# Optimization experiments

Hardware: AMD Instinct MI355X
Metric: run time of the kernel (lower is better)

The kernel has to match this reference:

```python
import jax, jax.numpy as jnp
import numpy as np

N_NODES = 50000
N_EDGES = 800000
D = 128           # 2 * hidden_channels
N_LAYERS = 9
N_GRAPHS = 256
EPS = 1e-05


def setup_inputs() -> dict:
    key = jax.random.key(0)
    ks = jax.random.split(key, 12)
    x = jax.random.normal(ks[0], (N_NODES, 13), dtype=jnp.float32)
    edge_index = jax.random.randint(ks[1], (2, N_EDGES), 0, N_NODES, dtype=jnp.int64)
    edge_attr = jax.random.normal(ks[2], (N_EDGES, 4), dtype=jnp.float32)
    batch = jnp.sort(jax.random.randint(ks[3], (N_NODES,), 0, N_GRAPHS, dtype=jnp.int64))
    s13 = 1.0 / np.sqrt(13)
    s4 = 1.0 / np.sqrt(4)
    sD = 1.0 / np.sqrt(D)
    s512 = 1.0 / np.sqrt(512)
    Wv = jax.random.uniform(ks[4], (13, D), jnp.float32, -s13, s13)
    We = jax.random.uniform(ks[5], (4, D), jnp.float32, -s4, s4)
    conv_w = jax.random.uniform(ks[6], (N_LAYERS, D, D), jnp.float32, -sD, sD)
    conv_b = jax.random.uniform(ks[7], (N_LAYERS, D), jnp.float32, -sD, sD)
    Wh1 = jax.random.uniform(ks[8], (D, 512), jnp.float32, -sD, sD)
    bh1 = jax.random.uniform(ks[9], (512,), jnp.float32, -sD, sD)
    Wh2 = jax.random.uniform(ks[10], (512, 1), jnp.float32, -s512, s512)
    bh2 = jax.random.uniform(ks[11], (1,), jnp.float32, -s512, s512)
    return {"x": x, "edge_index": edge_index, "edge_attr": edge_attr, "batch": batch,
            "Wv": Wv, "We": We, "conv_w": conv_w, "conv_b": conv_b,
            "Wh1": Wh1, "bh1": bh1, "Wh2": Wh2, "bh2": bh2}


def reference(x, edge_index, edge_attr, batch, Wv, We, conv_w, conv_b, Wh1, bh1, Wh2, bh2):
    src, dst = edge_index[0], edge_index[1]
    h = x @ Wv                      # [N, D]
    ea = edge_attr @ We             # [E, D]

    def layer(h, wb):
        W, b = wb
        msg = jax.nn.relu(h[src] + ea)                     # [E, D] gather + elementwise
        aggr = jax.ops.segment_sum(msg, dst, num_segments=N_NODES)  # scatter-add
        out = ((1.0 + EPS) * h + aggr) @ W + b             # GINEConv nn (Linear)
        return jax.nn.relu(out) + h, None                  # residual

    h, _ = jax.lax.scan(layer, h, (conv_w, conv_b))

    # global mean pool over graphs
    sums = jax.ops.segment_sum(h, batch, num_segments=N_GRAPHS)    # [G, D]
    cnt = jax.ops.segment_sum(jnp.ones((h.shape[0],), h.dtype), batch, num_segments=N_GRAPHS)
    pooled = sums / jnp.maximum(cnt, 1.0)[:, None]

    out = jax.nn.gelu(pooled @ Wh1 + bh1, approximate=False) @ Wh2 + bh2  # [G, 1]
    return out
```

## Files before the change

kernel.cpp:

```cpp
#include <hip/hip_runtime.h>
#include <math.h>

#define N_NODES 50000
#define N_EDGES 800000
#define DCH 128
#define N_LAYERS 9
#define N_GRAPHS 256
#define EPSF 1e-5f
#define NCHUNK 196
#define NSLICE 4
#define SL_SZ 12500

typedef __attribute__((ext_vector_type(8))) short short8;
typedef __attribute__((ext_vector_type(4))) float floatx4;

static __device__ __forceinline__ unsigned short f2bf(float f) {
    unsigned int u = __float_as_uint(f);
    unsigned int r = (u + 0x7fffu + ((u >> 16) & 1u)) >> 16;
    return (unsigned short)r;
}
static __device__ __forceinline__ unsigned int pack_bf2(float a, float b) {
    return (unsigned int)f2bf(a) | ((unsigned int)f2bf(b) << 16);
}
static __device__ __forceinline__ float bflo(unsigned int u) { return __uint_as_float(u << 16); }
static __device__ __forceinline__ float bfhi(unsigned int u) { return __uint_as_float(u & 0xffff0000u); }

static __device__ __forceinline__ float dot2bf(unsigned int a, unsigned int b, float c) {
    float d;
    asm("v_dot2_f32_bf16 %0, %1, %2, %3" : "=v"(d) : "v"(a), "v"(b), "v"(c));
    return d;
}

static __device__ __forceinline__ int dbucket(int d) { return 63 - min(d, 63); }

__global__ void hist_kernel(const int* __restrict__ dst, int* __restrict__ deg) {
    int t = blockIdx.x * 256 + threadIdx.x;
    atomicAdd(&deg[dst[t]], 1);
}

__global__ __launch_bounds__(256) void dsort_hist_kernel(const int* __restrict__ deg,
                                                         int* __restrict__ bhist) {
    __shared__ int lh[64];
    int t = threadIdx.x;
    if (t < 64) lh[t] = 0;
    __syncthreads();
    int n = blockIdx.x * 256 + t;
    if (n < N_NODES) atomicAdd(&lh[dbucket(deg[n])], 1);
    __syncthreads();
    if (t < 64) bhist[blockIdx.x * 64 + t] = lh[t];
}

__global__ __launch_bounds__(64) void dsort_scan_kernel(const int* __restrict__ bhist,
                                                        int* __restrict__ boff) {
    __shared__ int tot[64];
    __shared__ int base[64];
    int b = threadIdx.x;
    int s = 0;
    for (int blk = 0; blk < NCHUNK; blk++) s += bhist[blk * 64 + b];
    tot[b] = s;
    __syncthreads();
    if (b == 0) {
        int run = 0;
        for (int i = 0; i < 64; i++) { base[i] = run; run += tot[i]; }
    }
    __syncthreads();
    int run = base[b];
    for (int blk = 0; blk < NCHUNK; blk++) {
        boff[blk * 64 + b] = run;
        run += bhist[blk * 64 + b];
    }
}

__global__ __launch_bounds__(256) void dsort_scatter_kernel(const int* __restrict__ deg,
                                                            const int* __restrict__ boff,
                                                            int* __restrict__ nperm,
                                                            int* __restrict__ inv) {
    __shared__ int cur[64];
    int t = threadIdx.x;
    if (t < 64) cur[t] = boff[blockIdx.x * 64 + t];
    __syncthreads();
    int n = blockIdx.x * 256 + t;
    if (n < N_NODES) {
        int p = atomicAdd(&cur[dbucket(deg[n])], 1);
        nperm[p] = n;
        inv[n] = p;
    }
}

__global__ void dstinv_kernel(const int* __restrict__ dst, const int* __restrict__ inv,
                              int* __restrict__ dstinv) {
    int t = blockIdx.x * 256 + threadIdx.x;
    dstinv[t] = inv[dst[t]];
}

__global__ __launch_bounds__(256) void chunksum_kernel(const int* __restrict__ deg,
                                                       const int* __restrict__ nperm,
                                                       int* __restrict__ csum) {
    int t = threadIdx.x;
    int i = blockIdx.x * 256 + t;
    int v = (i < N_NODES) ? deg[nperm[i]] : 0;
    __shared__ int sh[4];
    for (int off = 32; off >= 1; off >>= 1) v += __shfl_down(v, off);
    if ((t & 63) == 0) sh[t >> 6] = v;
    __syncthreads();
    if (t == 0) csum[blockIdx.x] = sh[0] + sh[1] + sh[2] + sh[3];
}

__global__ __launch_bounds__(256) void chunkscan_kernel(const int* __restrict__ csum,
                                                        int* __restrict__ coff) {
    __shared__ int sh[256];
    int t = threadIdx.x;
    sh[t] = (t < NCHUNK) ? csum[t] : 0;
    __syncthreads();
    for (int off = 1; off < 256; off <<= 1) {
        int v = (t >= off) ? sh[t - off] : 0;
        __syncthreads();
        sh[t] += v;
        __syncthreads();
    }
    if (t < NCHUNK) coff[t] = t ? sh[t - 1] : 0;
}

__global__ __launch_bounds__(256) void applyscan_kernel(const int* __restrict__ deg,
                                                        const int* __restrict__ nperm,
                                                        const int* __restrict__ coff,
                                                        int* __restrict__ rowp,
                                                        int* __restrict__ cursor) {
    __shared__ int sh[256];
    int t = threadIdx.x;
    int i = blockIdx.x * 256 + t;
    int d = (i < N_NODES) ? deg[nperm[i]] : 0;
    sh[t] = d;
    __syncthreads();
    for (int off = 1; off < 256; off <<= 1) {
        int v = (t >= off) ? sh[t - off] : 0;
        __syncthreads();
        sh[t] += v;
        __syncthreads();
    }
    int excl = coff[blockIdx.x] + (t ? sh[t - 1] : 0);
    if (i < N_NODES) {
        rowp[i] = excl;
        cursor[i] = excl;
    }
    if (i == N_NODES - 1) rowp[N_NODES] = N_EDGES;
}

__global__ __launch_bounds__(256) void scatter_kernel(const int* __restrict__ src,
                                                      const int* __restrict__ dstinv,
                                                      const int* __restrict__ inv,
                                                      const float* __restrict__ eattr,
                                                      int* __restrict__ cursor,
                                                      uint4* __restrict__ erec) {
    int s = blockIdx.x & (NSLICE - 1);
    int chunk = blockIdx.x / NSLICE;
    int e0 = chunk * 1024 + threadIdx.x * 4;
    if (e0 >= N_EDGES) return;
    int4 d4 = *(const int4*)(dstinv + e0);
#pragma unroll
    for (int k = 0; k < 4; k++) {
        int e = e0 + k;
        int d = (k == 0) ? d4.x : (k == 1) ? d4.y : (k == 2) ? d4.z : d4.w;
        if (d / SL_SZ == s) {
            int p = atomicAdd(&cursor[d], 1);
            float4 a = ((const float4*)eattr)[e];
            erec[p] = make_uint4((unsigned int)inv[src[e]],
                                 pack_bf2(a.x, a.y), pack_bf2(a.z, a.w), 0u);
        }
    }
}

__global__ __launch_bounds__(256) void wconv_kernel(const float* __restrict__ convW,
                                                    uint4* __restrict__ wb) {
    int tid = blockIdx.x * 256 + threadIdx.x;
    int lane = tid & 63;
    int t = (tid >> 6) & 31;
    int layer = tid >> 11;
    int jt = t >> 2, kt = t & 3;
    int quad = lane >> 4, col = lane & 15;
    const float* Wl = convW + (size_t)layer * DCH * DCH;
    int kbase = kt * 32 + quad * 8;
    int ch = jt * 16 + col;
    unsigned int d0 = pack_bf2(Wl[(kbase + 0) * DCH + ch], Wl[(kbase + 1) * DCH + ch]);
    unsigned int d1 = pack_bf2(Wl[(kbase + 2) * DCH + ch], Wl[(kbase + 3) * DCH + ch]);
    unsigned int d2 = pack_bf2(Wl[(kbase + 4) * DCH + ch], Wl[(kbase + 5) * DCH + ch]);
    unsigned int d3 = pack_bf2(Wl[(kbase + 6) * DCH + ch], Wl[(kbase + 7) * DCH + ch]);
    wb[tid] = make_uint4(d0, d1, d2, d3);
}

__global__ void h0_kernel(const float* __restrict__ x, const float* __restrict__ Wv,
                          const int* __restrict__ inv,
                          float* __restrict__ h, unsigned int* __restrict__ hbf) {
    int t = blockIdx.x * 256 + threadIdx.x;
    int n = t >> 6, l = t & 63;
    const float* xr = x + n * 13;
    float s0 = 0.f, s1 = 0.f;
#pragma unroll
    for (int j = 0; j < 13; j++) {
        float xv = xr[j];
        s0 = fmaf(xv, Wv[j * 128 + 2 * l], s0);
        s1 = fmaf(xv, Wv[j * 128 + 2 * l + 1], s1);
    }
    int p = inv[n];
    ((float2*)h)[(size_t)p * 64 + l] = make_float2(s0, s1);
    hbf[(size_t)p * 64 + l] = pack_bf2(s0, s1);
}

#define VSTRIDE 68
#define OLP 132
__global__ __launch_bounds__(256) void layer_kernel(const float* __restrict__ hin,
                                                    const unsigned int* __restrict__ hbfA,
                                                    const uint4* __restrict__ erec,
                                                    const int* __restrict__ rowp,
                                                    const float* __restrict__ We,
                                                    const short8* __restrict__ wbL,
                                                    const float* __restrict__ b,
                                                    float* __restrict__ hout,
                                                    unsigned int* __restrict__ hbfB,
                                                    int write_hbf) {
    __shared__ unsigned int vsh[16 * VSTRIDE];
    __shared__ float ol[16 * OLP];
    __shared__ float2 hsh[16 * 64];
    int tid = threadIdx.x;
    int lane = tid & 63;
    int wave = tid >> 6;
    int nb = blockIdx.x * 16;
    unsigned int wy0 = pack_bf2(We[0 * 128 + 2 * lane], We[1 * 128 + 2 * lane]);
    unsigned int wz0 = pack_bf2(We[2 * 128 + 2 * lane], We[3 * 128 + 2 * lane]);
    unsigned int wy1 = pack_bf2(We[0 * 128 + 2 * lane + 1], We[1 * 128 + 2 * lane + 1]);
    unsigned int wz1 = pack_bf2(We[2 * 128 + 2 * lane + 1], We[3 * 128 + 2 * lane + 1]);
    const float2* h2 = (const float2*)hin;
    for (int j = 0; j < 4; j++) {
        int nl = wave * 4 + j;
        int n = nb + nl;
        int start = rowp[n], end = rowp[n + 1];
        float a0 = 0.f, a1 = 0.f;
        int e = start;
        for (; e + 4 <= end; e += 4) {
            uint4 r0 = erec[e], r1 = erec[e + 1], r2 = erec[e + 2], r3 = erec[e + 3];
            unsigned int u0 = hbfA[r0.x * 64u + (unsigned)lane];
            unsigned int u1 = hbfA[r1.x * 64u + (unsigned)lane];
            unsigned int u2 = hbfA[r2.x * 64u + (unsigned)lane];
            unsigned int u3 = hbfA[r3.x * 64u + (unsigned)lane];
            float p0 = dot2bf(r0.y, wy0, dot2bf(r0.z, wz0, 0.f));
            float p1 = dot2bf(r0.y, wy1, dot2bf(r0.z, wz1, 0.f));
            float q0 = dot2bf(r1.y, wy0, dot2bf(r1.z, wz0, 0.f));
            float q1 = dot2bf(r1.y, wy1, dot2bf(r1.z, wz1, 0.f));
            float s0 = dot2bf(r2.y, wy0, dot2bf(r2.z, wz0, 0.f));
            float s1 = dot2bf(r2.y, wy1, dot2bf(r2.z, wz1, 0.f));
            float t0 = dot2bf(r3.y, wy0, dot2bf(r3.z, wz0, 0.f));
            float t1 = dot2bf(r3.y, wy1, dot2bf(r3.z, wz1, 0.f));
            a0 += fmaxf(bflo(u0) + p0, 0.f);
            a1 += fmaxf(bfhi(u0) + p1, 0.f);
            a0 += fmaxf(bflo(u1) + q0, 0.f);
            a1 += fmaxf(bfhi(u1) + q1, 0.f);
            a0 += fmaxf(bflo(u2) + s0, 0.f);
            a1 += fmaxf(bfhi(u2) + s1, 0.f);
            a0 += fmaxf(bflo(u3) + t0, 0.f);
            a1 += fmaxf(bfhi(u3) + t1, 0.f);
        }
        for (; e < end; e++) {
            uint4 r0 = erec[e];
            unsigned int u0 = hbfA[r0.x * 64u + (unsigned)lane];
            float p0 = dot2bf(r0.y, wy0, dot2bf(r0.z, wz0, 0.f));
            float p1 = dot2bf(r0.y, wy1, dot2bf(r0.z, wz1, 0.f));
            a0 += fmaxf(bflo(u0) + p0, 0.f);
            a1 += fmaxf(bfhi(u0) + p1, 0.f);
        }
        float2 hn = h2[(size_t)n * 64 + lane];
        hsh[nl * 64 + lane] = hn;
        float vx = fmaf(hn.x, 1.f + EPSF, a0);
        float vy = fmaf(hn.y, 1.f + EPSF, a1);
        vsh[nl * VSTRIDE + lane] = pack_bf2(vx, vy);
    }
    __syncthreads();
    int col = lane & 15, quad = lane >> 4;
    short8 a[4];
#pragma unroll
    for (int kt = 0; kt < 4; kt++) {
        a[kt] = *(const short8*)(vsh + col * VSTRIDE + kt * 16 + quad * 4);
    }
#pragma unroll
    for (int jj = 0; jj < 2; jj++) {
        int jt = wave * 2 + jj;
        floatx4 acc = {0.f, 0.f, 0.f, 0.f};
#pragma unroll
        for (int kt = 0; kt < 4; kt++) {
            short8 bf = wbL[(jt * 4 + kt) * 64 + lane];
            acc = __builtin_amdgcn_mfma_f32_16x16x32_bf16(a[kt], bf, acc, 0, 0, 0);
        }
        float bv = b[jt * 16 + col];
#pragma unroll
        for (int r = 0; r < 4; r++) {
            ol[(quad * 4 + r) * OLP + jt * 16 + col] = fmaxf(acc[r] + bv, 0.f);
        }
    }
    __syncthreads();
    float4* o4 = (float4*)hout;
    uint2* b2 = (uint2*)hbfB;
#pragma unroll
    for (int i = 0; i < 2; i++) {
        int idx = i * 256 + tid;
        int nl = idx >> 5, c4 = idx & 31;
        int node = nb + nl;
        const float* row = ol + nl * OLP + c4 * 4;
        float2 h01 = hsh[nl * 64 + 2 * c4];
        float2 h23 = hsh[nl * 64 + 2 * c4 + 1];
        float4 r;
        r.x = row[0] + h01.x;
        r.y = row[1] + h01.y;
        r.z = row[2] + h23.x;
        r.w = row[3] + h23.y;
        o4[(size_t)node * 32 + c4] = r;
        if (write_hbf)
            b2[(size_t)node * 32 + c4] = make_uint2(pack_bf2(r.x, r.y), pack_bf2(r.z, r.w));
    }
}

__global__ void bounds_kernel(const int* __restrict__ batch, int* __restrict__ gs) {
    int n = blockIdx.x * 256 + threadIdx.x;
    if (n >= N_NODES) return;
    int bcur = batch[n];
    int prev = (n == 0) ? -1 : batch[n - 1];
    for (int g = prev + 1; g <= bcur; g++) gs[g] = n;
    if (n == N_NODES - 1) {
        for (int g = bcur + 1; g <= N_GRAPHS; g++) gs[g] = N_NODES;
    }
}

__global__ __launch_bounds__(256) void pool_kernel(const float* __restrict__ h,
                                                   const int* __restrict__ inv,
                                                   const int* __restrict__ batch,
                                                   float* __restrict__ sums) {
    int wave = threadIdx.x >> 6, l = threadIdx.x & 63;
    int nbase = (blockIdx.x * 4 + wave) * 8;
    const float2* h2 = (const float2*)h;
    float a0 = 0.f, a1 = 0.f;
    int g = -1;
#pragma unroll
    for (int i = 0; i < 8; i++) {
        int n = nbase + i;
        if (n >= N_NODES) break;
        int bg = batch[n];
        if (bg != g) {
            if (g >= 0) {
                atomicAdd(&sums[g * 128 + 2 * l], a0);
                atomicAdd(&sums[g * 128 + 2 * l + 1], a1);
            }
            g = bg; a0 = 0.f; a1 = 0.f;
        }
        int p = inv[n];
        float2 hv = h2[(size_t)p * 64 + l];
        a0 += hv.x; a1 += hv.y;
    }
    if (g >= 0) {
        atomicAdd(&sums[g * 128 + 2 * l], a0);
        atomicAdd(&sums[g * 128 + 2 * l + 1], a1);
    }
}

__global__ __launch_bounds__(512) void mlp_kernel(const float* __restrict__ sums,
                                                  const int* __restrict__ gs,
                                                  const float* __restrict__ Wh1,
                                                  const float* __restrict__ bh1,
                                                  const float* __restrict__ Wh2,
                                                  const float* __restrict__ bh2,
                                                  float* __restrict__ out) {
    int g = blockIdx.x;
    __shared__ float pl[128];
    __shared__ float red[8];
    int tid = threadIdx.x;
    if (tid < 128) {
        float cnt = fmaxf((float)(gs[g + 1] - gs[g]), 1.0f);
        pl[tid] = sums[g * 128 + tid] / cnt;
    }
    __syncthreads();
    float s = bh1[tid];
#pragma unroll 16
    for (int k = 0; k < 128; k++) s = fmaf(pl[k], Wh1[k * 512 + tid], s);
    float gl = 0.5f * s * (1.0f + erff(s * 0.70710678118654752f));
    float p = gl * Wh2[tid];
    for (int off = 32; off >= 1; off >>= 1) p += __shfl_down(p, off);
    if ((tid & 63) == 0) red[tid >> 6] = p;
    __syncthreads();
    if (tid == 0) {
        float tot = 0.f;
        for (int i = 0; i < 8; i++) tot += red[i];
        out[g] = tot + bh2[0];
    }
}

extern "C" void kernel_launch(void* const* d_in, const int* in_sizes, int n_in,
                              void* d_out, int out_size, void* d_ws, size_t ws_size,
                              hipStream_t stream) {
    const float* x = (const float*)d_in[0];
    const int* ei = (const int*)d_in[1];
    const float* eattr = (const float*)d_in[2];
    const int* batch = (const int*)d_in[3];
    const float* Wv = (const float*)d_in[4];
    const float* We = (const float*)d_in[5];
    const float* convW = (const float*)d_in[6];
    const float* convB = (const float*)d_in[7];
    const float* Wh1 = (const float*)d_in[8];
    const float* bh1 = (const float*)d_in[9];
    const float* Wh2 = (const float*)d_in[10];
    const float* bh2 = (const float*)d_in[11];
    float* out = (float*)d_out;

    const int* src = ei;
    const int* dst = ei + N_EDGES;

    char* w = (char*)d_ws;
    size_t off = 0;
    auto alloc = [&](size_t bytes) -> char* {
        char* p = w + off;
        off += (bytes + 255) & ~(size_t)255;
        return p;
    };
    float* bufA = (float*)alloc((size_t)N_NODES * DCH * 4);
    float* bufB = (float*)alloc((size_t)N_NODES * DCH * 4);
    unsigned int* hbfA = (unsigned int*)alloc((size_t)N_NODES * 64 * 4);
    unsigned int* hbfB = (unsigned int*)alloc((size_t)N_NODES * 64 * 4);
    uint4* wb = (uint4*)alloc((size_t)N_LAYERS * 32 * 64 * 16);
    int* deg = (int*)alloc((size_t)(N_NODES + 1) * 4);
    int* rowp = (int*)alloc((size_t)(N_NODES + 1) * 4);
    int* cursor = (int*)alloc((size_t)(N_NODES + 1) * 4);
    int* csum = (int*)alloc((size_t)NCHUNK * 4);
    int* coff = (int*)alloc((size_t)NCHUNK * 4);
    int* bhist = (int*)alloc((size_t)NCHUNK * 64 * 4);
    int* boff = (int*)alloc((size_t)NCHUNK * 64 * 4);
    int* nperm = (int*)alloc((size_t)N_NODES * 4);
    int* inv = (int*)alloc((size_t)N_NODES * 4);
    int* dstinv = (int*)alloc((size_t)N_EDGES * 4);
    uint4* erec = (uint4*)alloc((size_t)N_EDGES * 16);
    int* gs = (int*)alloc((size_t)(N_GRAPHS + 1) * 4);
    float* sums = (float*)alloc((size_t)N_GRAPHS * DCH * 4);
    (void)ws_size; (void)n_in; (void)in_sizes; (void)out_size;

    hipMemsetAsync(deg, 0, (size_t)(N_NODES + 1) * 4, stream);
    hipMemsetAsync(sums, 0, (size_t)N_GRAPHS * DCH * 4, stream);

    hist_kernel<<<N_EDGES / 256, 256, 0, stream>>>(dst, deg);
    dsort_hist_kernel<<<NCHUNK, 256, 0, stream>>>(deg, bhist);
    dsort_scan_kernel<<<1, 64, 0, stream>>>(bhist, boff);
    dsort_scatter_kernel<<<NCHUNK, 256, 0, stream>>>(deg, boff, nperm, inv);
    dstinv_kernel<<<N_EDGES / 256, 256, 0, stream>>>(dst, inv, dstinv);
    chunksum_kernel<<<NCHUNK, 256, 0, stream>>>(deg, nperm, csum);
    chunkscan_kernel<<<1, 256, 0, stream>>>(csum, coff);
    applyscan_kernel<<<NCHUNK, 256, 0, stream>>>(deg, nperm, coff, rowp, cursor);
    scatter_kernel<<<782 * NSLICE, 256, 0, stream>>>(src, dstinv, inv, eattr, cursor, erec);
    wconv_kernel<<<72, 256, 0, stream>>>(convW, wb);
    h0_kernel<<<N_NODES * 64 / 256, 256, 0, stream>>>(x, Wv, inv, bufA, hbfA);
    bounds_kernel<<<(N_NODES + 255) / 256, 256, 0, stream>>>(batch, gs);

    float* hcur = bufA;
    float* hnext = bufB;
    unsigned int* bfcur = hbfA;
    unsigned int* bfnext = hbfB;
    for (int layer = 0; layer < N_LAYERS; layer++) {
        layer_kernel<<<N_NODES / 16, 256, 0, stream>>>(
            hcur, bfcur, erec, rowp, We,
            (const short8*)(wb + (size_t)layer * 2048), convB + (size_t)layer * DCH,
            hnext, bfnext, (layer < N_LAYERS - 1) ? 1 : 0);
        float* t = hcur; hcur = hnext; hnext = t;
        unsigned int* tb = bfcur; bfcur = bfnext; bfnext = tb;
    }

    pool_kernel<<<(N_NODES + 31) / 32, 256, 0, stream>>>(hcur, inv, batch, sums);
    mlp_kernel<<<N_GRAPHS, 512, 0, stream>>>(sums, gs, Wh1, bh1, Wh2, bh2, out);
}
```

Baseline: 696.1 us.

## Flatten per-wave edge loop across four nodes with 8-wide prefetched gathers

Each wave now walks the concatenated edge range of its four destination nodes as one stream, processing 8 edges per iteration and prefetching the next 8 edge records while the current gathers are in flight. Accumulators are flushed into shared memory whenever a node boundary is crossed. Row pointers go through readfirstlane and the four h rows are loaded up front. Launch bounds now request 5 blocks per CU. The goal is more memory-level parallelism and less tail-loop overhead for low-degree nodes, at the cost of higher register pressure and per-edge boundary checks.

```diff
diff --git a/kernel.cpp b/kernel.cpp
--- a/kernel.cpp
+++ b/kernel.cpp
@@ -208,16 +208,16 @@
 
 #define VSTRIDE 68
 #define OLP 132
-__global__ __launch_bounds__(256) void layer_kernel(const float* __restrict__ hin,
-                                                    const unsigned int* __restrict__ hbfA,
-                                                    const uint4* __restrict__ erec,
-                                                    const int* __restrict__ rowp,
-                                                    const float* __restrict__ We,
-                                                    const short8* __restrict__ wbL,
-                                                    const float* __restrict__ b,
-                                                    float* __restrict__ hout,
-                                                    unsigned int* __restrict__ hbfB,
-                                                    int write_hbf) {
+__global__ __launch_bounds__(256, 5) void layer_kernel(const float* __restrict__ hin,
+                                                       const unsigned int* __restrict__ hbfA,
+                                                       const uint4* __restrict__ erec,
+                                                       const int* __restrict__ rowp,
+                                                       const float* __restrict__ We,
+                                                       const short8* __restrict__ wbL,
+                                                       const float* __restrict__ b,
+                                                       float* __restrict__ hout,
+                                                       unsigned int* __restrict__ hbfB,
+                                                       int write_hbf) {
     __shared__ unsigned int vsh[16 * VSTRIDE];
     __shared__ float ol[16 * OLP];
     __shared__ float2 hsh[16 * 64];
@@ -230,49 +230,95 @@
     unsigned int wy1 = pack_bf2(We[0 * 128 + 2 * lane + 1], We[1 * 128 + 2 * lane + 1]);
     unsigned int wz1 = pack_bf2(We[2 * 128 + 2 * lane + 1], We[3 * 128 + 2 * lane + 1]);
     const float2* h2 = (const float2*)hin;
-    for (int j = 0; j < 4; j++) {
-        int nl = wave * 4 + j;
-        int n = nb + nl;
-        int start = rowp[n], end = rowp[n + 1];
-        float a0 = 0.f, a1 = 0.f;
-        int e = start;
-        for (; e + 4 <= end; e += 4) {
-            uint4 r0 = erec[e], r1 = erec[e + 1], r2 = erec[e + 2], r3 = erec[e + 3];
-            unsigned int u0 = hbfA[r0.x * 64u + (unsigned)lane];
-            unsigned int u1 = hbfA[r1.x * 64u + (unsigned)lane];
-            unsigned int u2 = hbfA[r2.x * 64u + (unsigned)lane];
-            unsigned int u3 = hbfA[r3.x * 64u + (unsigned)lane];
-            float p0 = dot2bf(r0.y, wy0, dot2bf(r0.z, wz0, 0.f));
-            float p1 = dot2bf(r0.y, wy1, dot2bf(r0.z, wz1, 0.f));
-            float q0 = dot2bf(r1.y, wy0, dot2bf(r1.z, wz0, 0.f));
-            float q1 = dot2bf(r1.y, wy1, dot2bf(r1.z, wz1, 0.f));
-            float s0 = dot2bf(r2.y, wy0, dot2bf(r2.z, wz0, 0.f));
-            float s1 = dot2bf(r2.y, wy1, dot2bf(r2.z, wz1, 0.f));
-            float t0 = dot2bf(r3.y, wy0, dot2bf(r3.z, wz0, 0.f));
-            float t1 = dot2bf(r3.y, wy1, dot2bf(r3.z, wz1, 0.f));
-            a0 += fmaxf(bflo(u0) + p0, 0.f);
-            a1 += fmaxf(bfhi(u0) + p1, 0.f);
-            a0 += fmaxf(bflo(u1) + q0, 0.f);
-            a1 += fmaxf(bfhi(u1) + q1, 0.f);
-            a0 += fmaxf(bflo(u2) + s0, 0.f);
-            a1 += fmaxf(bfhi(u2) + s1, 0.f);
-            a0 += fmaxf(bflo(u3) + t0, 0.f);
-            a1 += fmaxf(bfhi(u3) + t1, 0.f);
+
+    int n0 = nb + wave * 4;
+    int b0 = __builtin_amdgcn_readfirstlane(rowp[n0]);
+    int b1 = __builtin_amdgcn_readfirstlane(rowp[n0 + 1]);
+    int b2 = __builtin_amdgcn_readfirstlane(rowp[n0 + 2]);
+    int b3 = __builtin_amdgcn_readfirstlane(rowp[n0 + 3]);
+    int b4 = __builtin_amdgcn_readfirstlane(rowp[n0 + 4]);
+
+    float2 hn0 = h2[(size_t)(n0 + 0) * 64 + lane];
+    float2 hn1 = h2[(size_t)(n0 + 1) * 64 + lane];
+    float2 hn2 = h2[(size_t)(n0 + 2) * 64 + lane];
+    float2 hn3 = h2[(size_t)(n0 + 3) * 64 + lane];
+    hsh[(wave * 4 + 0) * 64 + lane] = hn0;
+    hsh[(wave * 4 + 1) * 64 + lane] = hn1;
+    hsh[(wave * 4 + 2) * 64 + lane] = hn2;
+    hsh[(wave * 4 + 3) * 64 + lane] = hn3;
+
+    float c0 = 0.f, c1 = 0.f;
+    int nl = 0;
+    int bq = b1;
+
+    auto FLUSH = [&]() {
+        float hx = (nl == 0) ? hn0.x : (nl == 1) ? hn1.x : (nl == 2) ? hn2.x : hn3.x;
+        float hy = (nl == 0) ? hn0.y : (nl == 1) ? hn1.y : (nl == 2) ? hn2.y : hn3.y;
+        float vx = fmaf(hx, 1.f + EPSF, c0);
+        float vy = fmaf(hy, 1.f + EPSF, c1);
+        vsh[(wave * 4 + nl) * VSTRIDE + lane] = pack_bf2(vx, vy);
+        c0 = 0.f;
+        c1 = 0.f;
+        nl++;
+        bq = (nl == 1) ? b2 : (nl == 2) ? b3 : b4;
+    };
+
+    int cnt = b4 - b0;
+    int efull = b0 + (cnt & ~7);
+    int e = b0;
+
+    uint4 ra0, ra1, ra2, ra3, ra4, ra5, ra6, ra7;
+    if (e < efull) {
+        ra0 = erec[e + 0]; ra1 = erec[e + 1]; ra2 = erec[e + 2]; ra3 = erec[e + 3];
+        ra4 = erec[e + 4]; ra5 = erec[e + 5]; ra6 = erec[e + 6]; ra7 = erec[e + 7];
+    }
+    while (e < efull) {
+        unsigned int u0 = hbfA[ra0.x * 64u + (unsigned)lane];
+        unsigned int u1 = hbfA[ra1.x * 64u + (unsigned)lane];
+        unsigned int u2 = hbfA[ra2.x * 64u + (unsigned)lane];
+        unsigned int u3 = hbfA[ra3.x * 64u + (unsigned)lane];
+        unsigned int u4 = hbfA[ra4.x * 64u + (unsigned)lane];
+        unsigned int u5 = hbfA[ra5.x * 64u + (unsigned)lane];
+        unsigned int u6 = hbfA[ra6.x * 64u + (unsigned)lane];
+        unsigned int u7 = hbfA[ra7.x * 64u + (unsigned)lane];
+        unsigned int y0 = ra0.y, z0 = ra0.z, y1 = ra1.y, z1 = ra1.z;
+        unsigned int y2 = ra2.y, z2 = ra2.z, y3 = ra3.y, z3 = ra3.z;
+        unsigned int y4 = ra4.y, z4 = ra4.z, y5 = ra5.y, z5 = ra5.z;
+        unsigned int y6 = ra6.y, z6 = ra6.z, y7 = ra7.y, z7 = ra7.z;
+        if (e + 8 < efull) {
+            ra0 = erec[e + 8]; ra1 = erec[e + 9]; ra2 = erec[e + 10]; ra3 = erec[e + 11];
+            ra4 = erec[e + 12]; ra5 = erec[e + 13]; ra6 = erec[e + 14]; ra7 = erec[e + 15];
         }
-        for (; e < end; e++) {
-            uint4 r0 = erec[e];
-            unsigned int u0 = hbfA[r0.x * 64u + (unsigned)lane];
-            float p0 = dot2bf(r0.y, wy0, dot2bf(r0.z, wz0, 0.f));
-            float p1 = dot2bf(r0.y, wy1, dot2bf(r0.z, wz1, 0.f));
-            a0 += fmaxf(bflo(u0) + p0, 0.f);
-            a1 += fmaxf(bfhi(u0) + p1, 0.f);
+#define EDGE(K, UK, YK, ZK)                                                   \
+        {                                                                     \
+            while (e + K == bq) FLUSH();                                      \
+            float m0 = dot2bf(YK, wy0, dot2bf(ZK, wz0, 0.f));                 \
+            float m1 = dot2bf(YK, wy1, dot2bf(ZK, wz1, 0.f));                 \
+            c0 += fmaxf(bflo(UK) + m0, 0.f);                                  \
+            c1 += fmaxf(bfhi(UK) + m1, 0.f);                                  \
         }
-        float2 hn = h2[(size_t)n * 64 + lane];
-        hsh[nl * 64 + lane] = hn;
-        float vx = fmaf(hn.x, 1.f + EPSF, a0);
-        float vy = fmaf(hn.y, 1.f + EPSF, a1);
-        vsh[nl * VSTRIDE + lane] = pack_bf2(vx, vy);
-    }
+        EDGE(0, u0, y0, z0)
+        EDGE(1, u1, y1, z1)
+        EDGE(2, u2, y2, z2)
+        EDGE(3, u3, y3, z3)
+        EDGE(4, u4, y4, z4)
+        EDGE(5, u5, y5, z5)
+        EDGE(6, u6, y6, z6)
+        EDGE(7, u7, y7, z7)
+#undef EDGE
+        e += 8;
+    }
+    for (; e < b4; e++) {
+        while (e == bq) FLUSH();
+        uint4 r0 = erec[e];
+        unsigned int uu = hbfA[r0.x * 64u + (unsigned)lane];
+        float m0 = dot2bf(r0.y, wy0, dot2bf(r0.z, wz0, 0.f));
+        float m1 = dot2bf(r0.y, wy1, dot2bf(r0.z, wz1, 0.f));
+        c0 += fmaxf(bflo(uu) + m0, 0.f);
+        c1 += fmaxf(bfhi(uu) + m1, 0.f);
+    }
+    while (nl < 4) FLUSH();
+
     __syncthreads();
     int col = lane & 15, quad = lane >> 4;
     short8 a[4];
@@ -297,15 +343,15 @@
     }
     __syncthreads();
     float4* o4 = (float4*)hout;
-    uint2* b2 = (uint2*)hbfB;
+    uint2* b2v = (uint2*)hbfB;
 #pragma unroll
     for (int i = 0; i < 2; i++) {
         int idx = i * 256 + tid;
-        int nl = idx >> 5, c4 = idx & 31;
-        int node = nb + nl;
-        const float* row = ol + nl * OLP + c4 * 4;
-        float2 h01 = hsh[nl * 64 + 2 * c4];
-        float2 h23 = hsh[nl * 64 + 2 * c4 + 1];
+        int nl2 = idx >> 5, c4 = idx & 31;
+        int node = nb + nl2;
+        const float* row = ol + nl2 * OLP + c4 * 4;
+        float2 h01 = hsh[nl2 * 64 + 2 * c4];
+        float2 h23 = hsh[nl2 * 64 + 2 * c4 + 1];
         float4 r;
         r.x = row[0] + h01.x;
         r.y = row[1] + h01.y;
@@ -313,7 +359,7 @@
         r.w = row[3] + h23.y;
         o4[(size_t)node * 32 + c4] = r;
         if (write_hbf)
-            b2[(size_t)node * 32 + c4] = make_uint2(pack_bf2(r.x, r.y), pack_bf2(r.z, r.w));
+            b2v[(size_t)node * 32 + c4] = make_uint2(pack_bf2(r.x, r.y), pack_bf2(r.z, r.w));
     }
 }
 
```

Result: slower. 1.019 ms (+46.4%).

## Interleave edge gathers across four nodes per wave with software-prefetched edge records

Applied to the files above, without the earlier changes.

Each wave now processes its four destination nodes together, looping to the maximum degree among them and masking inactive slots, so four independent neighbor gathers are in flight per iteration instead of handling nodes one after another. Edge records for the next iteration are prefetched with clamped indices, and the node feature loads are hoisted ahead of the loop. The aim is more memory-level parallelism to hide gather latency. In exchange, nodes with unequal degrees waste work on masked iterations, and register pressure rises.

```diff
diff --git a/kernel.cpp b/kernel.cpp
--- a/kernel.cpp
+++ b/kernel.cpp
@@ -230,49 +230,76 @@
     unsigned int wy1 = pack_bf2(We[0 * 128 + 2 * lane + 1], We[1 * 128 + 2 * lane + 1]);
     unsigned int wz1 = pack_bf2(We[2 * 128 + 2 * lane + 1], We[3 * 128 + 2 * lane + 1]);
     const float2* h2 = (const float2*)hin;
-    for (int j = 0; j < 4; j++) {
-        int nl = wave * 4 + j;
-        int n = nb + nl;
-        int start = rowp[n], end = rowp[n + 1];
-        float a0 = 0.f, a1 = 0.f;
-        int e = start;
-        for (; e + 4 <= end; e += 4) {
-            uint4 r0 = erec[e], r1 = erec[e + 1], r2 = erec[e + 2], r3 = erec[e + 3];
-            unsigned int u0 = hbfA[r0.x * 64u + (unsigned)lane];
-            unsigned int u1 = hbfA[r1.x * 64u + (unsigned)lane];
-            unsigned int u2 = hbfA[r2.x * 64u + (unsigned)lane];
-            unsigned int u3 = hbfA[r3.x * 64u + (unsigned)lane];
-            float p0 = dot2bf(r0.y, wy0, dot2bf(r0.z, wz0, 0.f));
-            float p1 = dot2bf(r0.y, wy1, dot2bf(r0.z, wz1, 0.f));
-            float q0 = dot2bf(r1.y, wy0, dot2bf(r1.z, wz0, 0.f));
-            float q1 = dot2bf(r1.y, wy1, dot2bf(r1.z, wz1, 0.f));
-            float s0 = dot2bf(r2.y, wy0, dot2bf(r2.z, wz0, 0.f));
-            float s1 = dot2bf(r2.y, wy1, dot2bf(r2.z, wz1, 0.f));
-            float t0 = dot2bf(r3.y, wy0, dot2bf(r3.z, wz0, 0.f));
-            float t1 = dot2bf(r3.y, wy1, dot2bf(r3.z, wz1, 0.f));
-            a0 += fmaxf(bflo(u0) + p0, 0.f);
-            a1 += fmaxf(bfhi(u0) + p1, 0.f);
-            a0 += fmaxf(bflo(u1) + q0, 0.f);
-            a1 += fmaxf(bfhi(u1) + q1, 0.f);
-            a0 += fmaxf(bflo(u2) + s0, 0.f);
-            a1 += fmaxf(bfhi(u2) + s1, 0.f);
-            a0 += fmaxf(bflo(u3) + t0, 0.f);
-            a1 += fmaxf(bfhi(u3) + t1, 0.f);
+
+    int n0 = nb + wave * 4;
+    int s0 = __builtin_amdgcn_readfirstlane(rowp[n0]);
+    int s1 = __builtin_amdgcn_readfirstlane(rowp[n0 + 1]);
+    int s2 = __builtin_amdgcn_readfirstlane(rowp[n0 + 2]);
+    int s3 = __builtin_amdgcn_readfirstlane(rowp[n0 + 3]);
+    int s4 = __builtin_amdgcn_readfirstlane(rowp[n0 + 4]);
+    int d0 = s1 - s0, d1 = s2 - s1, d2 = s3 - s2, d3 = s4 - s3;
+    int dm0 = d0 - 1, dm1 = d1 - 1, dm2 = d2 - 1, dm3 = d3 - 1;
+    int maxd = max(max(d0, d1), max(d2, d3));
+    int mm = maxd - 1;
+
+    float2 hn0 = h2[(size_t)(n0 + 0) * 64 + lane];
+    float2 hn1 = h2[(size_t)(n0 + 1) * 64 + lane];
+    float2 hn2 = h2[(size_t)(n0 + 2) * 64 + lane];
+    float2 hn3 = h2[(size_t)(n0 + 3) * 64 + lane];
+    hsh[(wave * 4 + 0) * 64 + lane] = hn0;
+    hsh[(wave * 4 + 1) * 64 + lane] = hn1;
+    hsh[(wave * 4 + 2) * 64 + lane] = hn2;
+    hsh[(wave * 4 + 3) * 64 + lane] = hn3;
+
+    float c0x = 0.f, c0y = 0.f, c1x = 0.f, c1y = 0.f;
+    float c2x = 0.f, c2y = 0.f, c3x = 0.f, c3y = 0.f;
+
+    if (maxd > 0) {
+        uint4 q0 = erec[s0 + min(0, dm0)];
+        uint4 q1 = erec[s1 + min(0, dm1)];
+        uint4 q2 = erec[s2 + min(0, dm2)];
+        uint4 q3 = erec[s3 + min(0, dm3)];
+        for (int i = 0; i < maxd; i++) {
+            unsigned int u0 = hbfA[q0.x * 64u + (unsigned)lane];
+            unsigned int u1 = hbfA[q1.x * 64u + (unsigned)lane];
+            unsigned int u2 = hbfA[q2.x * 64u + (unsigned)lane];
+            unsigned int u3 = hbfA[q3.x * 64u + (unsigned)lane];
+            unsigned int y0 = q0.y, z0 = q0.z;
+            unsigned int y1 = q1.y, z1 = q1.z;
+            unsigned int y2 = q2.y, z2 = q2.z;
+            unsigned int y3 = q3.y, z3 = q3.z;
+            int inx = min(i + 1, mm);
+            q0 = erec[s0 + min(inx, dm0)];
+            q1 = erec[s1 + min(inx, dm1)];
+            q2 = erec[s2 + min(inx, dm2)];
+            q3 = erec[s3 + min(inx, dm3)];
+            float m00 = dot2bf(y0, wy0, dot2bf(z0, wz0, 0.f));
+            float m01 = dot2bf(y0, wy1, dot2bf(z0, wz1, 0.f));
+            float m10 = dot2bf(y1, wy0, dot2bf(z1, wz0, 0.f));
+            float m11 = dot2bf(y1, wy1, dot2bf(z1, wz1, 0.f));
+            float m20 = dot2bf(y2, wy0, dot2bf(z2, wz0, 0.f));
+            float m21 = dot2bf(y2, wy1, dot2bf(z2, wz1, 0.f));
+            float m30 = dot2bf(y3, wy0, dot2bf(z3, wz0, 0.f));
+            float m31 = dot2bf(y3, wy1, dot2bf(z3, wz1, 0.f));
+            c0x += (i < d0) ? fmaxf(bflo(u0) + m00, 0.f) : 0.f;
+            c0y += (i < d0) ? fmaxf(bfhi(u0) + m01, 0.f) : 0.f;
+            c1x += (i < d1) ? fmaxf(bflo(u1) + m10, 0.f) : 0.f;
+            c1y += (i < d1) ? fmaxf(bfhi(u1) + m11, 0.f) : 0.f;
+            c2x += (i < d2) ? fmaxf(bflo(u2) + m20, 0.f) : 0.f;
+            c2y += (i < d2) ? fmaxf(bfhi(u2) + m21, 0.f) : 0.f;
+            c3x += (i < d3) ? fmaxf(bflo(u3) + m30, 0.f) : 0.f;
+            c3y += (i < d3) ? fmaxf(bfhi(u3) + m31, 0.f) : 0.f;
         }
-        for (; e < end; e++) {
-            uint4 r0 = erec[e];
-            unsigned int u0 = hbfA[r0.x * 64u + (unsigned)lane];
-            float p0 = dot2bf(r0.y, wy0, dot2bf(r0.z, wz0, 0.f));
-            float p1 = dot2bf(r0.y, wy1, dot2bf(r0.z, wz1, 0.f));
-            a0 += fmaxf(bflo(u0) + p0, 0.f);
-            a1 += fmaxf(bfhi(u0) + p1, 0.f);
-        }
-        float2 hn = h2[(size_t)n * 64 + lane];
-        hsh[nl * 64 + lane] = hn;
-        float vx = fmaf(hn.x, 1.f + EPSF, a0);
-        float vy = fmaf(hn.y, 1.f + EPSF, a1);
-        vsh[nl * VSTRIDE + lane] = pack_bf2(vx, vy);
-    }
+    }
+    vsh[(wave * 4 + 0) * VSTRIDE + lane] =
+        pack_bf2(fmaf(hn0.x, 1.f + EPSF, c0x), fmaf(hn0.y, 1.f + EPSF, c0y));
+    vsh[(wave * 4 + 1) * VSTRIDE + lane] =
+        pack_bf2(fmaf(hn1.x, 1.f + EPSF, c1x), fmaf(hn1.y, 1.f + EPSF, c1y));
+    vsh[(wave * 4 + 2) * VSTRIDE + lane] =
+        pack_bf2(fmaf(hn2.x, 1.f + EPSF, c2x), fmaf(hn2.y, 1.f + EPSF, c2y));
+    vsh[(wave * 4 + 3) * VSTRIDE + lane] =
+        pack_bf2(fmaf(hn3.x, 1.f + EPSF, c3x), fmaf(hn3.y, 1.f + EPSF, c3y));
+
     __syncthreads();
     int col = lane & 15, quad = lane >> 4;
     short8 a[4];
@@ -297,15 +324,15 @@
     }
     __syncthreads();
     float4* o4 = (float4*)hout;
-    uint2* b2 = (uint2*)hbfB;
+    uint2* b2v = (uint2*)hbfB;
 #pragma unroll
     for (int i = 0; i < 2; i++) {
         int idx = i * 256 + tid;
-        int nl = idx >> 5, c4 = idx & 31;
-        int node = nb + nl;
-        const float* row = ol + nl * OLP + c4 * 4;
-        float2 h01 = hsh[nl * 64 + 2 * c4];
-        float2 h23 = hsh[nl * 64 + 2 * c4 + 1];
+        int nl2 = idx >> 5, c4 = idx & 31;
+        int node = nb + nl2;
+        const float* row = ol + nl2 * OLP + c4 * 4;
+        float2 h01 = hsh[nl2 * 64 + 2 * c4];
+        float2 h23 = hsh[nl2 * 64 + 2 * c4 + 1];
         float4 r;
         r.x = row[0] + h01.x;
         r.y = row[1] + h01.y;
@@ -313,7 +340,7 @@
         r.w = row[3] + h23.y;
         o4[(size_t)node * 32 + c4] = r;
         if (write_hbf)
-            b2[(size_t)node * 32 + c4] = make_uint2(pack_bf2(r.x, r.y), pack_bf2(r.z, r.w));
+            b2v[(size_t)node * 32 + c4] = make_uint2(pack_bf2(r.x, r.y), pack_bf2(r.z, r.w));
     }
 }
 
```

After: 629.5 us. -9.6%, faster.
